# Kernel optimization log

Measured on AMD Instinct MI355X. Metric: run time of the kernel, lower is better.

## Reference

```python
import jax, jax.numpy as jnp
import numpy as np
import math

N_HEADS = 16
DIM = 1024
D_HEAD = DIM // N_HEADS
BS, QLEN = 2, 2048


def setup_inputs() -> dict:
    key = jax.random.key(0)
    ks = jax.random.split(key, 10)
    s = 0.02
    return {
        "input": jax.random.normal(ks[0], (BS, QLEN, DIM), dtype=jnp.float32),
        "mask": jnp.ones((BS, QLEN), dtype=jnp.int32),
        "q_w": jax.random.normal(ks[1], (DIM, DIM), dtype=jnp.float32) * s,
        "q_b": jax.random.normal(ks[2], (DIM,), dtype=jnp.float32) * s,
        "k_w": jax.random.normal(ks[3], (DIM, DIM), dtype=jnp.float32) * s,
        "k_b": jax.random.normal(ks[4], (DIM,), dtype=jnp.float32) * s,
        "v_w": jax.random.normal(ks[5], (DIM, DIM), dtype=jnp.float32) * s,
        "v_b": jax.random.normal(ks[6], (DIM,), dtype=jnp.float32) * s,
        "o_w": jax.random.normal(ks[7], (DIM, DIM), dtype=jnp.float32) * s,
        "o_b": jax.random.normal(ks[8], (DIM,), dtype=jnp.float32) * s,
    }


def _shape(x, bs):
    # (bs, len, dim) -> (bs, heads, len, d_head)
    return x.reshape(bs, -1, N_HEADS, D_HEAD).transpose(0, 2, 1, 3)


def reference(input, mask, q_w, q_b, k_w, k_b, v_w, v_b, o_w, o_b):
    bs, qlen, dim = input.shape
    # projections (torch Linear: x @ W^T + b)
    q = _shape(input @ q_w.T + q_b, bs)
    k = _shape(input @ k_w.T + k_b, bs)
    v = _shape(input @ v_w.T + v_b, bs)
    q = q / math.sqrt(D_HEAD)
    # scores: (bs, heads, qlen, klen)
    scores = jnp.einsum("bhqd,bhkd->bhqk", q, k)
    pad = (mask == 0)[:, None, None, :]  # (bs,1,1,klen)
    scores = jnp.where(pad, -jnp.inf, scores)
    weights = jax.nn.softmax(scores.astype(jnp.float32), axis=-1).astype(scores.dtype)
    # dropout p=0.0 (eval) -> identity
    context = jnp.einsum("bhqk,bhkd->bhqd", weights, v)
    context = context.transpose(0, 2, 1, 3).reshape(bs, qlen, dim)
    return context @ o_w.T + o_b
```

## Files before the change

### kernel.cpp

```cpp
#include <hip/hip_runtime.h>


#define BS    2
#define QLEN  2048
#define DIM   1024
#define NH    16
#define DH    64
#define MTOK  (BS * QLEN)

#define QSCALE 0.18033688011112042f

typedef __attribute__((ext_vector_type(8))) short short8;
typedef __attribute__((ext_vector_type(4))) float float4_t;
typedef __attribute__((ext_vector_type(4))) int   int4_t;

__device__ __forceinline__ ushort f2bf(float f) {
    unsigned u = __float_as_uint(f);
    return (ushort)((u + 0x7fffu + ((u >> 16) & 1u)) >> 16);
}
__device__ __forceinline__ short8 pack8(float4 a0, float4 a1) {
    short8 r;
    r[0] = (short)f2bf(a0.x); r[1] = (short)f2bf(a0.y);
    r[2] = (short)f2bf(a0.z); r[3] = (short)f2bf(a0.w);
    r[4] = (short)f2bf(a1.x); r[5] = (short)f2bf(a1.y);
    r[6] = (short)f2bf(a1.z); r[7] = (short)f2bf(a1.w);
    return r;
}

__device__ __forceinline__ void glds16(const void* g, void* l) {
    __builtin_amdgcn_global_load_lds(
        (const __attribute__((address_space(1))) unsigned int*)g,
        (__attribute__((address_space(3))) unsigned int*)l, 16, 0, 0);
}

__global__ __launch_bounds__(256) void conv_all(
    const float* __restrict__ x,  const float* __restrict__ qw,
    const float* __restrict__ kw, const float* __restrict__ vw,
    const float* __restrict__ ow,
    ushort* __restrict__ Xbf, ushort* __restrict__ Wbf)
{
    const int blk = blockIdx.x;
    const float* s; ushort* d; size_t base;
    if (blk < 4096)      { s = x;  d = Xbf;             base = (size_t)blk * 1024; }
    else if (blk < 5120) { s = qw; d = Wbf;             base = (size_t)(blk - 4096) * 1024; }
    else if (blk < 6144) { s = kw; d = Wbf + 1048576;   base = (size_t)(blk - 5120) * 1024; }
    else if (blk < 7168) { s = vw; d = Wbf + 2097152;   base = (size_t)(blk - 6144) * 1024; }
    else                 { s = ow; d = Wbf + 3145728;   base = (size_t)(blk - 7168) * 1024; }
    const size_t i = base + threadIdx.x * 4;
    float4 v = *(const float4*)(s + i);
    ushort4 o;
    o.x = f2bf(v.x); o.y = f2bf(v.y); o.z = f2bf(v.z); o.w = f2bf(v.w);
    *(ushort4*)(d + i) = o;
}

__global__ __launch_bounds__(256) void transpose_v(
    const ushort* __restrict__ Vrow, ushort* __restrict__ Vt)
{
    __shared__ ushort T[64][72];
    const int tid  = threadIdx.x;
    const int tile = blockIdx.x;
    const int bh   = blockIdx.y;
    const int b = bh >> 4, h = bh & 15;

    #pragma unroll
    for (int rep = 0; rep < 2; ++rep) {
        int ch = tid + rep * 256;
        int tok = ch >> 3, seg = ch & 7;
        uint4 v = *(const uint4*)(Vrow + (size_t)(b * QLEN + tile * 64 + tok) * DIM
                                        + h * DH + seg * 8);
        *(uint4*)&T[tok][seg * 8] = v;
    }
    __syncthreads();
    #pragma unroll
    for (int rep = 0; rep < 2; ++rep) {
        int ch = tid + rep * 256;
        int dim = ch >> 3, tseg = ch & 7;
        ushort t0 = T[tseg * 8 + 0][dim], t1 = T[tseg * 8 + 1][dim];
        ushort t2 = T[tseg * 8 + 2][dim], t3 = T[tseg * 8 + 3][dim];
        ushort t4 = T[tseg * 8 + 4][dim], t5 = T[tseg * 8 + 5][dim];
        ushort t6 = T[tseg * 8 + 6][dim], t7 = T[tseg * 8 + 7][dim];
        uint4 o;
        o.x = (unsigned)t0 | ((unsigned)t1 << 16);
        o.y = (unsigned)t2 | ((unsigned)t3 << 16);
        o.z = (unsigned)t4 | ((unsigned)t5 << 16);
        o.w = (unsigned)t6 | ((unsigned)t7 << 16);
        *(uint4*)(Vt + (size_t)bh * DH * QLEN + (size_t)dim * QLEN
                      + tile * 64 + tseg * 8) = o;
    }
}

__global__ __launch_bounds__(256) void gemm_qkv(
    const ushort* __restrict__ A, const ushort* __restrict__ Bw,
    const float* __restrict__ bias0, const float* __restrict__ bias1,
    const float* __restrict__ bias2,
    ushort* __restrict__ outQ, ushort* __restrict__ outK, ushort* __restrict__ outVt)
{
    __shared__ ushort As[2][128 * 32];
    __shared__ ushort Bs[2][128 * 32];
    const int tid  = threadIdx.x;
    const int w    = tid >> 6;
    const int lane = tid & 63;
    const int r15  = lane & 15;
    const int quad = lane >> 4;
    const int xcd = blockIdx.x & 7;
    const int lid = blockIdx.x >> 3;
    const int brow = (xcd & 3) * 8  + (lid & 7);
    const int bcol = (xcd >> 2) * 12 + (lid >> 3);
    const int wrow = (w >> 1) * 64;
    const int wcol = (w & 1) * 64;
    const int K = DIM;

    float4_t acc[4][4];
    #pragma unroll
    for (int i = 0; i < 4; ++i)
        #pragma unroll
        for (int j = 0; j < 4; ++j)
            acc[i][j] = (float4_t){0.f, 0.f, 0.f, 0.f};

    int chS[2];
    const ushort* gaS[2];
    const ushort* gbS[2];
    #pragma unroll
    for (int rep = 0; rep < 2; ++rep) {
        const int ch  = w * 128 + rep * 64 + lane;
        const int row = ch >> 2;
        const int g   = (ch & 3) ^ ((row >> 1) & 3);
        chS[rep] = ch;
        gaS[rep] = A  + (size_t)(brow * 128 + row) * K + g * 8;
        gbS[rep] = Bw + (size_t)(bcol * 128 + row) * K + g * 8;
    }
    const int ph = (quad ^ ((r15 >> 1) & 3)) * 8;

    #pragma unroll
    for (int rep = 0; rep < 2; ++rep) {
        glds16(gaS[rep], &As[0][chS[rep] * 8]);
        glds16(gbS[rep], &Bs[0][chS[rep] * 8]);
    }
    __syncthreads();

    int p = 0;
    for (int k0 = 0; k0 < K; k0 += 32) {
        if (k0 + 32 < K) {
            #pragma unroll
            for (int rep = 0; rep < 2; ++rep) {
                glds16(gaS[rep] + k0 + 32, &As[p ^ 1][chS[rep] * 8]);
                glds16(gbS[rep] + k0 + 32, &Bs[p ^ 1][chS[rep] * 8]);
            }
        }
        short8 af[4], bf[4];
        #pragma unroll
        for (int ms = 0; ms < 4; ++ms)
            af[ms] = *(const short8*)&As[p][(wrow + ms * 16 + r15) * 32 + ph];
        #pragma unroll
        for (int ns = 0; ns < 4; ++ns)
            bf[ns] = *(const short8*)&Bs[p][(wcol + ns * 16 + r15) * 32 + ph];
        #pragma unroll
        for (int ms = 0; ms < 4; ++ms)
            #pragma unroll
            for (int ns = 0; ns < 4; ++ns)
                acc[ms][ns] = __builtin_amdgcn_mfma_f32_16x16x32_bf16(
                    af[ms], bf[ns], acc[ms][ns], 0, 0, 0);
        __syncthreads();
        p ^= 1;
    }

    #pragma unroll
    for (int ms = 0; ms < 4; ++ms) {
        const int rowg = brow * 128 + wrow + ms * 16 + quad * 4;
        #pragma unroll
        for (int ns = 0; ns < 4; ++ns) {
            const int colg = bcol * 128 + wcol + ns * 16 + r15;
            if (colg < 1024) {
                const float bb = bias0[colg];
                #pragma unroll
                for (int r = 0; r < 4; ++r)
                    outQ[(size_t)(rowg + r) * 1024 + colg] =
                        f2bf((acc[ms][ns][r] + bb) * QSCALE);
            } else if (colg < 2048) {
                const float bb = bias1[colg - 1024];
                #pragma unroll
                for (int r = 0; r < 4; ++r)
                    outK[(size_t)(rowg + r) * 1024 + (colg - 1024)] =
                        f2bf(acc[ms][ns][r] + bb);
            } else {
                const int vcol = colg - 2048;
                const int hh = vcol >> 6, dd = vcol & 63;
                const float bb = bias2[vcol];
                const int bidx = rowg >> 11;
                const int tloc = rowg & 2047;
                ushort4 o4;
                o4.x = f2bf(acc[ms][ns][0] + bb);
                o4.y = f2bf(acc[ms][ns][1] + bb);
                o4.z = f2bf(acc[ms][ns][2] + bb);
                o4.w = f2bf(acc[ms][ns][3] + bb);
                *(ushort4*)&outVt[((size_t)(bidx * 16 + hh) * 64 + dd) * QLEN + tloc] = o4;
            }
        }
    }
}

__global__ __launch_bounds__(256) void gemm_o(
    const ushort* __restrict__ A, const ushort* __restrict__ Bw,
    const float* __restrict__ bias, float* __restrict__ Out)
{
    __shared__ ushort As[2][128 * 64];
    __shared__ ushort Bs[2][64 * 64];
    const int tid  = threadIdx.x;
    const int w    = tid >> 6;
    const int lane = tid & 63;
    const int r15  = lane & 15;
    const int quad = lane >> 4;
    const int xcd = blockIdx.x & 7;
    const int lid = blockIdx.x >> 3;
    const int brow = (xcd & 3) * 8 + (lid & 7);
    const int bcol = (xcd >> 2) * 8 + (lid >> 3);
    const int wrow = w * 32;
    const int K = DIM;

    float4_t acc[2][4];
    #pragma unroll
    for (int i = 0; i < 2; ++i)
        #pragma unroll
        for (int j = 0; j < 4; ++j)
            acc[i][j] = (float4_t){0.f, 0.f, 0.f, 0.f};

    int chA[4];  const ushort* gaS[4];
    #pragma unroll
    for (int rep = 0; rep < 4; ++rep) {
        const int ch  = w * 256 + rep * 64 + lane;
        const int row = ch >> 3;
        const int g   = (ch & 7) ^ (row & 7);
        chA[rep] = ch;
        gaS[rep] = A + (size_t)(brow * 128 + row) * K + g * 8;
    }
    int chB[2];  const ushort* gbS[2];
    #pragma unroll
    for (int rep = 0; rep < 2; ++rep) {
        const int ch  = w * 128 + rep * 64 + lane;
        const int row = ch >> 3;
        const int g   = (ch & 7) ^ (row & 7);
        chB[rep] = ch;
        gbS[rep] = Bw + (size_t)(bcol * 64 + row) * K + g * 8;
    }
    const int xg = r15 & 7;

    #pragma unroll
    for (int rep = 0; rep < 4; ++rep)
        glds16(gaS[rep], &As[0][chA[rep] * 8]);
    #pragma unroll
    for (int rep = 0; rep < 2; ++rep)
        glds16(gbS[rep], &Bs[0][chB[rep] * 8]);
    __syncthreads();

    int p = 0;
    for (int k0 = 0; k0 < K; k0 += 64) {
        if (k0 + 64 < K) {
            #pragma unroll
            for (int rep = 0; rep < 4; ++rep)
                glds16(gaS[rep] + k0 + 64, &As[p ^ 1][chA[rep] * 8]);
            #pragma unroll
            for (int rep = 0; rep < 2; ++rep)
                glds16(gbS[rep] + k0 + 64, &Bs[p ^ 1][chB[rep] * 8]);
        }
        #pragma unroll
        for (int hh = 0; hh < 2; ++hh) {
            const int ph = ((hh * 4 + quad) ^ xg) * 8;
            short8 af[2], bf[4];
            #pragma unroll
            for (int ms = 0; ms < 2; ++ms)
                af[ms] = *(const short8*)&As[p][(wrow + ms * 16 + r15) * 64 + ph];
            #pragma unroll
            for (int ns = 0; ns < 4; ++ns)
                bf[ns] = *(const short8*)&Bs[p][(ns * 16 + r15) * 64 + ph];
            #pragma unroll
            for (int ms = 0; ms < 2; ++ms)
                #pragma unroll
                for (int ns = 0; ns < 4; ++ns)
                    acc[ms][ns] = __builtin_amdgcn_mfma_f32_16x16x32_bf16(
                        af[ms], bf[ns], acc[ms][ns], 0, 0, 0);
        }
        __syncthreads();
        p ^= 1;
    }

    #pragma unroll
    for (int ms = 0; ms < 2; ++ms) {
        const int rowg = brow * 128 + wrow + ms * 16 + quad * 4;
        #pragma unroll
        for (int ns = 0; ns < 4; ++ns) {
            const int colg = bcol * 64 + ns * 16 + r15;
            const float bb = bias[colg];
            #pragma unroll
            for (int r = 0; r < 4; ++r)
                Out[(size_t)(rowg + r) * 1024 + colg] = acc[ms][ns][r] + bb;
        }
    }
}

__global__ __launch_bounds__(256) void gemm_f32in_bf16out(
    const float* __restrict__ X, const float* __restrict__ W,
    const float* __restrict__ B, ushort* __restrict__ Out,
    int M, int N, int K, float scale)
{
    const int lane = threadIdx.x & 63;
    const int wid  = (blockIdx.x * blockDim.x + threadIdx.x) >> 6;
    const int tilesN = N >> 4;
    const int tm = wid / tilesN;
    const int tn = wid - tm * tilesN;
    const int r15  = lane & 15;
    const int quad = lane >> 4;

    const float* xp = X + (size_t)(tm * 16 + r15) * K + quad * 8;
    const float* wp = W + (size_t)(tn * 16 + r15) * K + quad * 8;

    float4_t acc = {0.f, 0.f, 0.f, 0.f};
    for (int k0 = 0; k0 < K; k0 += 32) {
        float4 a0 = *(const float4*)(xp + k0);
        float4 a1 = *(const float4*)(xp + k0 + 4);
        float4 b0 = *(const float4*)(wp + k0);
        float4 b1 = *(const float4*)(wp + k0 + 4);
        acc = __builtin_amdgcn_mfma_f32_16x16x32_bf16(pack8(a0, a1), pack8(b0, b1), acc, 0, 0, 0);
    }
    const int col  = tn * 16 + r15;
    const float bias = B[col];
    const int row0 = tm * 16 + quad * 4;
    #pragma unroll
    for (int r = 0; r < 4; ++r)
        Out[(size_t)(row0 + r) * N + col] = f2bf((acc[r] + bias) * scale);
}

__global__ __launch_bounds__(256) void gemm_bf16in_f32out(
    const ushort* __restrict__ X, const float* __restrict__ W,
    const float* __restrict__ B, float* __restrict__ Out,
    int M, int N, int K)
{
    const int lane = threadIdx.x & 63;
    const int wid  = (blockIdx.x * blockDim.x + threadIdx.x) >> 6;
    const int tilesN = N >> 4;
    const int tm = wid / tilesN;
    const int tn = wid - tm * tilesN;
    const int r15  = lane & 15;
    const int quad = lane >> 4;

    const ushort* xp = X + (size_t)(tm * 16 + r15) * K + quad * 8;
    const float*  wp = W + (size_t)(tn * 16 + r15) * K + quad * 8;

    float4_t acc = {0.f, 0.f, 0.f, 0.f};
    for (int k0 = 0; k0 < K; k0 += 32) {
        short8 a = *(const short8*)(xp + k0);
        float4 b0 = *(const float4*)(wp + k0);
        float4 b1 = *(const float4*)(wp + k0 + 4);
        acc = __builtin_amdgcn_mfma_f32_16x16x32_bf16(a, pack8(b0, b1), acc, 0, 0, 0);
    }
    const int col  = tn * 16 + r15;
    const float bias = B[col];
    const int row0 = tm * 16 + quad * 4;
    #pragma unroll
    for (int r = 0; r < 4; ++r)
        Out[(size_t)(row0 + r) * N + col] = acc[r] + bias;
}

__global__ __launch_bounds__(256, 2) void flash_attn(
    const ushort* __restrict__ Qb, const ushort* __restrict__ Kb,
    const ushort* __restrict__ Vt, const int* __restrict__ mask,
    ushort* __restrict__ Cb)
{
    __shared__ __align__(16) ushort Ks[2][64][64];
    __shared__ __align__(16) ushort Vs[4][64][64];
    __shared__ __align__(16) float  Mb[QLEN];

    const int tid  = threadIdx.x;
    const int w    = tid >> 6;
    const int lane = tid & 63;
    const int r15  = lane & 15;
    const int quad = lane >> 4;
    const int bh = blockIdx.y;
    const int b = bh >> 4, h = bh & 15;

    {
        const int4* m4 = (const int4*)(mask + b * QLEN);
        #pragma unroll
        for (int rep = 0; rep < 2; ++rep) {
            const int idx = tid + rep * 256;
            int4 mv = m4[idx];
            float4 o;
            o.x = mv.x ? 0.f : -INFINITY;
            o.y = mv.y ? 0.f : -INFINITY;
            o.z = mv.z ? 0.f : -INFINITY;
            o.w = mv.w ? 0.f : -INFINITY;
            *(float4*)&Mb[idx * 4] = o;
        }
    }

    const int qbase = blockIdx.x * 128 + w * 32;
    const ushort* qp = Qb + (size_t)(b * QLEN + qbase + r15) * DIM + h * DH + quad * 8;
    short8 qf[2][2];
    qf[0][0] = *(const short8*)(qp);
    qf[0][1] = *(const short8*)(qp + 32);
    qf[1][0] = *(const short8*)(qp + 16 * DIM);
    qf[1][1] = *(const short8*)(qp + 16 * DIM + 32);

    const ushort* kg = Kb + (size_t)b * QLEN * DIM + h * DH;
    const ushort* vg = Vt + (size_t)bh * DH * QLEN;

    const int a0 = tid >> 3, seg = tid & 7;
    const int krow0 = (((a0 & 7) >> 2) << 4) + (((a0 >> 3) & 3) << 2) + (a0 & 3);
    const int sK = (seg ^ (krow0 & 7)) << 3;
    const int sV = (seg ^ (a0 & 7)) << 3;
    const int xq = (quad ^ (r15 & 7)) << 3;

    float4_t o[2][4];
    float4_t ol[2];
    #pragma unroll
    for (int rg = 0; rg < 2; ++rg) {
        ol[rg] = (float4_t){0.f, 0.f, 0.f, 0.f};
        #pragma unroll
        for (int ds = 0; ds < 4; ++ds)
            o[rg][ds] = (float4_t){0.f, 0.f, 0.f, 0.f};
    }
    short8 ones8;
    #pragma unroll
    for (int i = 0; i < 8; ++i) ones8[i] = (short)0x3F80;

    uint4 kr0, kr1, vr0, vr1;
    int pkA[4][2][2], pkB[4][2][2];

#define LOAD_TILE(KT) do {                                                    \
    kr0 = *(const uint4*)(kg + (size_t)((KT) + a0     ) * DIM  + seg * 8);    \
    kr1 = *(const uint4*)(kg + (size_t)((KT) + a0 + 32) * DIM  + seg * 8);    \
    vr0 = *(const uint4*)(vg + (size_t)(a0     ) * QLEN + (KT) + seg * 8);    \
    vr1 = *(const uint4*)(vg + (size_t)(a0 + 32) * QLEN + (KT) + seg * 8);    \
} while (0)

#define STORE_TILE(KBUF, VBUF) do {                                           \
    *(uint4*)&Ks[KBUF][krow0     ][sK] = kr0;                                 \
    *(uint4*)&Ks[KBUF][krow0 + 32][sK] = kr1;                                 \
    *(uint4*)&Vs[VBUF][a0        ][sV] = vr0;                                 \
    *(uint4*)&Vs[VBUF][a0 + 32   ][sV] = vr1;                                 \
} while (0)

#define S_PHASE(KBUF, KT, PK) do {                                            \
    _Pragma("unroll")                                                         \
    for (int ks = 0; ks < 4; ++ks) {                                          \
        const ushort* krow = &Ks[KBUF][ks * 16 + r15][0];                     \
        short8 kf0 = *(const short8*)(krow + xq);                             \
        short8 kf1 = *(const short8*)(krow + (xq ^ 32));                      \
        const float4 mb = *(const float4*)&Mb[(KT) + ((ks >> 1) << 5)         \
                                              + (quad << 3) + ((ks & 1) << 2)]; \
        _Pragma("unroll")                                                     \
        for (int rg = 0; rg < 2; ++rg) {                                      \
            float4_t s = {0.f, 0.f, 0.f, 0.f};                                \
            s = __builtin_amdgcn_mfma_f32_16x16x32_bf16(kf0, qf[rg][0], s, 0, 0, 0); \
            s = __builtin_amdgcn_mfma_f32_16x16x32_bf16(kf1, qf[rg][1], s, 0, 0, 0); \
            unsigned u0 = __float_as_uint(__builtin_amdgcn_exp2f(s[0] + mb.x)); \
            unsigned u1 = __float_as_uint(__builtin_amdgcn_exp2f(s[1] + mb.y)); \
            unsigned u2 = __float_as_uint(__builtin_amdgcn_exp2f(s[2] + mb.z)); \
            unsigned u3 = __float_as_uint(__builtin_amdgcn_exp2f(s[3] + mb.w)); \
            PK[ks][rg][0] = __builtin_amdgcn_perm(u1, u0, 0x07060302);        \
            PK[ks][rg][1] = __builtin_amdgcn_perm(u3, u2, 0x07060302);        \
        }                                                                     \
    }                                                                         \
} while (0)

#define PV_PHASE(VBUF, PK) do {                                               \
    _Pragma("unroll")                                                         \
    for (int ck = 0; ck < 2; ++ck) {                                          \
        short8 vf[4];                                                         \
        _Pragma("unroll")                                                     \
        for (int ds = 0; ds < 4; ++ds)                                        \
            vf[ds] = *(const short8*)(&Vs[VBUF][ds * 16 + r15][0] + (xq ^ (ck << 5))); \
        _Pragma("unroll")                                                     \
        for (int rg = 0; rg < 2; ++rg) {                                      \
            int4_t pfi = { PK[2 * ck][rg][0], PK[2 * ck][rg][1],              \
                           PK[2 * ck + 1][rg][0], PK[2 * ck + 1][rg][1] };    \
            short8 pf = __builtin_bit_cast(short8, pfi);                      \
            _Pragma("unroll")                                                 \
            for (int ds = 0; ds < 4; ++ds)                                    \
                o[rg][ds] = __builtin_amdgcn_mfma_f32_16x16x32_bf16(          \
                    pf, vf[ds], o[rg][ds], 0, 0, 0);                          \
            ol[rg] = __builtin_amdgcn_mfma_f32_16x16x32_bf16(                 \
                pf, ones8, ol[rg], 0, 0, 0);                                  \
        }                                                                     \
    }                                                                         \
} while (0)

    LOAD_TILE(0);
    STORE_TILE(0, 0);
    LOAD_TILE(64);
    __syncthreads();
    S_PHASE(0, 0, pkA);
    STORE_TILE(1, 1);
    __syncthreads();
    LOAD_TILE(128);

    for (int kb = 0; kb < 1792; kb += 256) {
        S_PHASE(1, kb + 64, pkB);  PV_PHASE(0, pkA);
        STORE_TILE(0, 2); __syncthreads(); LOAD_TILE(kb + 192);
        S_PHASE(0, kb + 128, pkA); PV_PHASE(1, pkB);
        STORE_TILE(1, 3); __syncthreads(); LOAD_TILE(kb + 256);
        S_PHASE(1, kb + 192, pkB); PV_PHASE(2, pkA);
        STORE_TILE(0, 0); __syncthreads(); LOAD_TILE(kb + 320);
        S_PHASE(0, kb + 256, pkA); PV_PHASE(3, pkB);
        STORE_TILE(1, 1); __syncthreads(); LOAD_TILE(kb + 384);
    }

    S_PHASE(1, 1856, pkB); PV_PHASE(0, pkA);
    STORE_TILE(0, 2); __syncthreads(); LOAD_TILE(1984);
    S_PHASE(0, 1920, pkA); PV_PHASE(1, pkB);
    STORE_TILE(1, 3); __syncthreads();
    S_PHASE(1, 1984, pkB); PV_PHASE(2, pkA);
    PV_PHASE(3, pkB);

#undef LOAD_TILE
#undef STORE_TILE
#undef S_PHASE
#undef PV_PHASE

    #pragma unroll
    for (int rg = 0; rg < 2; ++rg) {
        #pragma unroll
        for (int r = 0; r < 4; ++r) {
            const float ir = 1.f / fmaxf(ol[rg][r], 1e-30f);
            const size_t rb = (size_t)(b * QLEN + qbase + rg * 16 + quad * 4 + r) * DIM
                              + h * DH;
            Cb[rb +  0 + r15] = f2bf(o[rg][0][r] * ir);
            Cb[rb + 16 + r15] = f2bf(o[rg][1][r] * ir);
            Cb[rb + 32 + r15] = f2bf(o[rg][2][r] * ir);
            Cb[rb + 48 + r15] = f2bf(o[rg][3][r] * ir);
        }
    }
}

extern "C" void kernel_launch(void* const* d_in, const int* in_sizes, int n_in,
                              void* d_out, int out_size, void* d_ws, size_t ws_size,
                              hipStream_t stream)
{
    const float* x    = (const float*)d_in[0];
    const int*   mask = (const int*)d_in[1];
    const float* q_w  = (const float*)d_in[2];
    const float* q_b  = (const float*)d_in[3];
    const float* k_w  = (const float*)d_in[4];
    const float* k_b  = (const float*)d_in[5];
    const float* v_w  = (const float*)d_in[6];
    const float* v_b  = (const float*)d_in[7];
    const float* o_w  = (const float*)d_in[8];
    const float* o_b  = (const float*)d_in[9];
    float* out = (float*)d_out;

    const size_t SEG = (size_t)MTOK * DIM;
    ushort* Qbf = (ushort*)d_out;
    ushort* Xbf = Qbf + SEG;
    ushort* Kb  = (ushort*)d_ws;
    ushort* Cb  = Kb + SEG;
    ushort* Vt  = Cb + SEG;
    ushort* Wbf = Vt + SEG;

    const bool big = ws_size >= (size_t)32 * 1024 * 1024;

    if (big) {
        conv_all<<<8192, 256, 0, stream>>>(x, q_w, k_w, v_w, o_w, Xbf, Wbf);
        gemm_qkv<<<(MTOK / 128) * (3072 / 128), 256, 0, stream>>>(
            Xbf, Wbf, q_b, k_b, v_b, Qbf, Kb, Vt);
        flash_attn<<<dim3(QLEN / 128, BS * NH), 256, 0, stream>>>(Qbf, Kb, Vt, mask, Cb);
        gemm_o<<<(MTOK / 128) * (DIM / 64), 256, 0, stream>>>(
            Cb, Wbf + 3 * (size_t)(DIM * DIM), o_b, out);
    } else {
        const int tiles   = (MTOK / 16) * (DIM / 16);
        const int gblocks = tiles / 4;
        gemm_f32in_bf16out<<<gblocks, 256, 0, stream>>>(x, q_w, q_b, Qbf, MTOK, DIM, DIM, QSCALE);
        gemm_f32in_bf16out<<<gblocks, 256, 0, stream>>>(x, k_w, k_b, Kb,  MTOK, DIM, DIM, 1.0f);
        gemm_f32in_bf16out<<<gblocks, 256, 0, stream>>>(x, v_w, v_b, Cb,  MTOK, DIM, DIM, 1.0f);
        transpose_v<<<dim3(QLEN / 64, BS * NH), 256, 0, stream>>>(Cb, Vt);
        flash_attn<<<dim3(QLEN / 128, BS * NH), 256, 0, stream>>>(Qbf, Kb, Vt, mask, Cb);
        gemm_bf16in_f32out<<<tiles / 4, 256, 0, stream>>>(Cb, o_w, o_b, out, MTOK, DIM, DIM);
    }
}
```

Baseline: 191.5 us.

## Enlarge flash-attention query tile and stage K/V via direct global-to-LDS loads

Measured after the change: 206.9 us. 8.0% more time.

```diff
diff --git a/kernel.cpp b/kernel.cpp
--- a/kernel.cpp
+++ b/kernel.cpp
@@ -360,13 +360,13 @@
         Out[(size_t)(row0 + r) * N + col] = acc[r] + bias;
 }
 
-__global__ __launch_bounds__(256, 2) void flash_attn(
+__global__ __launch_bounds__(256, 1) void flash_attn(
     const ushort* __restrict__ Qb, const ushort* __restrict__ Kb,
     const ushort* __restrict__ Vt, const int* __restrict__ mask,
     ushort* __restrict__ Cb)
 {
     __shared__ __align__(16) ushort Ks[2][64][64];
-    __shared__ __align__(16) ushort Vs[4][64][64];
+    __shared__ __align__(16) ushort Vs[2][64][64];
     __shared__ __align__(16) float  Mb[QLEN];
 
     const int tid  = threadIdx.x;
@@ -392,27 +392,42 @@
         }
     }
 
-    const int qbase = blockIdx.x * 128 + w * 32;
+    const int qbase = blockIdx.x * 256 + w * 64;
     const ushort* qp = Qb + (size_t)(b * QLEN + qbase + r15) * DIM + h * DH + quad * 8;
-    short8 qf[2][2];
-    qf[0][0] = *(const short8*)(qp);
-    qf[0][1] = *(const short8*)(qp + 32);
-    qf[1][0] = *(const short8*)(qp + 16 * DIM);
-    qf[1][1] = *(const short8*)(qp + 16 * DIM + 32);
+    short8 qf[4][2];
+    #pragma unroll
+    for (int rg = 0; rg < 4; ++rg) {
+        qf[rg][0] = *(const short8*)(qp + rg * 16 * DIM);
+        qf[rg][1] = *(const short8*)(qp + rg * 16 * DIM + 32);
+    }
 
     const ushort* kg = Kb + (size_t)b * QLEN * DIM + h * DH;
     const ushort* vg = Vt + (size_t)bh * DH * QLEN;
 
-    const int a0 = tid >> 3, seg = tid & 7;
-    const int krow0 = (((a0 & 7) >> 2) << 4) + (((a0 >> 3) & 3) << 2) + (a0 & 3);
-    const int sK = (seg ^ (krow0 & 7)) << 3;
-    const int sV = (seg ^ (a0 & 7)) << 3;
+    int cc0, cc1;
+    const ushort* gk[2];
+    const ushort* gv[2];
+    {
+        #pragma unroll
+        for (int rep = 0; rep < 2; ++rep) {
+            const int c   = (w * 2 + rep) * 64 + lane;
+            const int row = c >> 3, slot = c & 7;
+            const int sg  = slot ^ (row & 7);
+            const int r5  = row & 31;
+            const int tok = (row & 32) | (((r5 >> 3) & 1) << 4) | (((r5 >> 2) & 1) << 3)
+                          | (((r5 >> 4) & 1) << 2) | (r5 & 3);
+            if (rep == 0) cc0 = c; else cc1 = c;
+            gk[rep] = kg + (size_t)tok * DIM  + sg * 8;
+            gv[rep] = vg + (size_t)row * QLEN + sg * 8;
+        }
+    }
+
     const int xq = (quad ^ (r15 & 7)) << 3;
 
-    float4_t o[2][4];
-    float4_t ol[2];
-    #pragma unroll
-    for (int rg = 0; rg < 2; ++rg) {
+    float4_t o[4][4];
+    float4_t ol[4];
+    #pragma unroll
+    for (int rg = 0; rg < 4; ++rg) {
         ol[rg] = (float4_t){0.f, 0.f, 0.f, 0.f};
         #pragma unroll
         for (int ds = 0; ds < 4; ++ds)
@@ -422,21 +437,16 @@
     #pragma unroll
     for (int i = 0; i < 8; ++i) ones8[i] = (short)0x3F80;
 
-    uint4 kr0, kr1, vr0, vr1;
-    int pkA[4][2][2], pkB[4][2][2];
-
-#define LOAD_TILE(KT) do {                                                    \
-    kr0 = *(const uint4*)(kg + (size_t)((KT) + a0     ) * DIM  + seg * 8);    \
-    kr1 = *(const uint4*)(kg + (size_t)((KT) + a0 + 32) * DIM  + seg * 8);    \
-    vr0 = *(const uint4*)(vg + (size_t)(a0     ) * QLEN + (KT) + seg * 8);    \
-    vr1 = *(const uint4*)(vg + (size_t)(a0 + 32) * QLEN + (KT) + seg * 8);    \
+    int pkA[4][4][2], pkB[4][4][2];
+
+#define STAGE_K(BUF, KT) do {                                                 \
+    glds16(gk[0] + (size_t)(KT) * DIM, (ushort*)Ks[BUF] + cc0 * 8);           \
+    glds16(gk[1] + (size_t)(KT) * DIM, (ushort*)Ks[BUF] + cc1 * 8);           \
 } while (0)
 
-#define STORE_TILE(KBUF, VBUF) do {                                           \
-    *(uint4*)&Ks[KBUF][krow0     ][sK] = kr0;                                 \
-    *(uint4*)&Ks[KBUF][krow0 + 32][sK] = kr1;                                 \
-    *(uint4*)&Vs[VBUF][a0        ][sV] = vr0;                                 \
-    *(uint4*)&Vs[VBUF][a0 + 32   ][sV] = vr1;                                 \
+#define STAGE_V(BUF, KT) do {                                                 \
+    glds16(gv[0] + (KT), (ushort*)Vs[BUF] + cc0 * 8);                         \
+    glds16(gv[1] + (KT), (ushort*)Vs[BUF] + cc1 * 8);                         \
 } while (0)
 
 #define S_PHASE(KBUF, KT, PK) do {                                            \
@@ -448,7 +458,7 @@
         const float4 mb = *(const float4*)&Mb[(KT) + ((ks >> 1) << 5)         \
                                               + (quad << 3) + ((ks & 1) << 2)]; \
         _Pragma("unroll")                                                     \
-        for (int rg = 0; rg < 2; ++rg) {                                      \
+        for (int rg = 0; rg < 4; ++rg) {                                      \
             float4_t s = {0.f, 0.f, 0.f, 0.f};                                \
             s = __builtin_amdgcn_mfma_f32_16x16x32_bf16(kf0, qf[rg][0], s, 0, 0, 0); \
             s = __builtin_amdgcn_mfma_f32_16x16x32_bf16(kf1, qf[rg][1], s, 0, 0, 0); \
@@ -463,6 +473,7 @@
 } while (0)
 
 #define PV_PHASE(VBUF, PK) do {                                               \
+    __builtin_amdgcn_s_setprio(1);                                            \
     _Pragma("unroll")                                                         \
     for (int ck = 0; ck < 2; ++ck) {                                          \
         short8 vf[4];                                                         \
@@ -470,7 +481,7 @@
         for (int ds = 0; ds < 4; ++ds)                                        \
             vf[ds] = *(const short8*)(&Vs[VBUF][ds * 16 + r15][0] + (xq ^ (ck << 5))); \
         _Pragma("unroll")                                                     \
-        for (int rg = 0; rg < 2; ++rg) {                                      \
+        for (int rg = 0; rg < 4; ++rg) {                                      \
             int4_t pfi = { PK[2 * ck][rg][0], PK[2 * ck][rg][1],              \
                            PK[2 * ck + 1][rg][0], PK[2 * ck + 1][rg][1] };    \
             short8 pf = __builtin_bit_cast(short8, pfi);                      \
@@ -482,42 +493,38 @@
                 pf, ones8, ol[rg], 0, 0, 0);                                  \
         }                                                                     \
     }                                                                         \
+    __builtin_amdgcn_s_setprio(0);                                            \
 } while (0)
 
-    LOAD_TILE(0);
-    STORE_TILE(0, 0);
-    LOAD_TILE(64);
+    STAGE_K(0, 0); STAGE_V(0, 0); STAGE_K(1, 64);
     __syncthreads();
     S_PHASE(0, 0, pkA);
-    STORE_TILE(1, 1);
     __syncthreads();
-    LOAD_TILE(128);
-
-    for (int kb = 0; kb < 1792; kb += 256) {
-        S_PHASE(1, kb + 64, pkB);  PV_PHASE(0, pkA);
-        STORE_TILE(0, 2); __syncthreads(); LOAD_TILE(kb + 192);
-        S_PHASE(0, kb + 128, pkA); PV_PHASE(1, pkB);
-        STORE_TILE(1, 3); __syncthreads(); LOAD_TILE(kb + 256);
-        S_PHASE(1, kb + 192, pkB); PV_PHASE(2, pkA);
-        STORE_TILE(0, 0); __syncthreads(); LOAD_TILE(kb + 320);
-        S_PHASE(0, kb + 256, pkA); PV_PHASE(3, pkB);
-        STORE_TILE(1, 1); __syncthreads(); LOAD_TILE(kb + 384);
-    }
-
-    S_PHASE(1, 1856, pkB); PV_PHASE(0, pkA);
-    STORE_TILE(0, 2); __syncthreads(); LOAD_TILE(1984);
-    S_PHASE(0, 1920, pkA); PV_PHASE(1, pkB);
-    STORE_TILE(1, 3); __syncthreads();
-    S_PHASE(1, 1984, pkB); PV_PHASE(2, pkA);
-    PV_PHASE(3, pkB);
-
-#undef LOAD_TILE
-#undef STORE_TILE
+
+    for (int kb = 0; kb < 1856; kb += 128) {
+        STAGE_V(1, kb + 64); STAGE_K(0, kb + 128);
+        S_PHASE(1, kb + 64, pkB);
+        PV_PHASE(0, pkA);
+        __syncthreads();
+        STAGE_V(0, kb + 128); STAGE_K(1, kb + 192);
+        S_PHASE(0, kb + 128, pkA);
+        PV_PHASE(1, pkB);
+        __syncthreads();
+    }
+
+    STAGE_V(1, 1984);
+    S_PHASE(1, 1984, pkB);
+    PV_PHASE(0, pkA);
+    __syncthreads();
+    PV_PHASE(1, pkB);
+
+#undef STAGE_K
+#undef STAGE_V
 #undef S_PHASE
 #undef PV_PHASE
 
     #pragma unroll
-    for (int rg = 0; rg < 2; ++rg) {
+    for (int rg = 0; rg < 4; ++rg) {
         #pragma unroll
         for (int r = 0; r < 4; ++r) {
             const float ir = 1.f / fmaxf(ol[rg][r], 1e-30f);
@@ -561,7 +568,7 @@
         conv_all<<<8192, 256, 0, stream>>>(x, q_w, k_w, v_w, o_w, Xbf, Wbf);
         gemm_qkv<<<(MTOK / 128) * (3072 / 128), 256, 0, stream>>>(
             Xbf, Wbf, q_b, k_b, v_b, Qbf, Kb, Vt);
-        flash_attn<<<dim3(QLEN / 128, BS * NH), 256, 0, stream>>>(Qbf, Kb, Vt, mask, Cb);
+        flash_attn<<<dim3(QLEN / 256, BS * NH), 256, 0, stream>>>(Qbf, Kb, Vt, mask, Cb);
         gemm_o<<<(MTOK / 128) * (DIM / 64), 256, 0, stream>>>(
             Cb, Wbf + 3 * (size_t)(DIM * DIM), o_b, out);
     } else {
@@ -571,7 +578,7 @@
         gemm_f32in_bf16out<<<gblocks, 256, 0, stream>>>(x, k_w, k_b, Kb,  MTOK, DIM, DIM, 1.0f);
         gemm_f32in_bf16out<<<gblocks, 256, 0, stream>>>(x, v_w, v_b, Cb,  MTOK, DIM, DIM, 1.0f);
         transpose_v<<<dim3(QLEN / 64, BS * NH), 256, 0, stream>>>(Cb, Vt);
-        flash_attn<<<dim3(QLEN / 128, BS * NH), 256, 0, stream>>>(Qbf, Kb, Vt, mask, Cb);
+        flash_attn<<<dim3(QLEN / 256, BS * NH), 256, 0, stream>>>(Qbf, Kb, Vt, mask, Cb);
         gemm_bf16in_f32out<<<tiles / 4, 256, 0, stream>>>(Cb, o_w, o_b, out, MTOK, DIM, DIM);
     }
 }
```
